# Kernel optimization log

Hardware: AMD Instinct MI355X
Metric: run time of the kernel (lower is better)

## Reference

```python
import jax, jax.numpy as jnp
from jax import lax
import numpy as np

B, S, E = 512, 128, 300
NF = 100          # filters per kernel size
NUM_CLASSES = 5


def setup_inputs() -> dict:
    key = jax.random.key(0)
    ks = jax.random.split(key, 9)
    def w(k, shape, fan_in):
        bound = 1.0 / np.sqrt(fan_in)
        return jax.random.uniform(k, shape, jnp.float32, -bound, bound)
    return {
        "x":   jax.random.normal(ks[0], (B, 1, S, E), jnp.float32),
        # conv weights: [out_ch=NF, in_ch=1, kh, kw=E] (the 100 separate 1-channel
        # convs of each kernel size are stacked into one grouped weight tensor)
        "w3": w(ks[1], (NF, 1, 3, E), 3 * E),
        "b3": w(ks[2], (NF,), 3 * E),
        "w4": w(ks[3], (NF, 1, 4, E), 4 * E),
        "b4": w(ks[4], (NF,), 4 * E),
        "w5": w(ks[5], (NF, 1, 5, E), 5 * E),
        "b5": w(ks[6], (NF,), 5 * E),
        "Wfc": w(ks[7], (NUM_CLASSES, 3 * NF), 3 * NF),
        "bfc": w(ks[8], (NUM_CLASSES,), 3 * NF),
    }


def _branch(x, w, b, pad):
    # conv over [B,1,S,E] with kernel [NF,1,k,E]; width fully consumed -> out [B,NF,S',1]
    y = lax.conv_general_dilated(
        x, w, window_strides=(1, 1), padding=[(pad, pad), (0, 0)],
        dimension_numbers=("NCHW", "OIHW", "NCHW"))
    y = jax.nn.relu(y + b[None, :, None, None])
    # relu then global max-pool over the length dim == max over (S', 1)
    return jnp.max(y, axis=(2, 3))  # [B, NF]


def reference(x, w3, b3, w4, b4, w5, b5, Wfc, bfc):
    feats = jnp.concatenate(
        [_branch(x, w3, b3, 0),   # k=3, no padding
         _branch(x, w4, b4, 1),   # k=4, padding (1,0)
         _branch(x, w5, b5, 2)],  # k=5, padding (2,0)
        axis=1)                   # [B, 300]
    logits = feats @ Wfc.T + bfc  # dropout is identity in eval mode
    return jax.nn.log_softmax(logits, axis=1)
```

## Files before the change

### kernel.cpp

```cpp
#include <hip/hip_runtime.h>

typedef __bf16 bf16x8 __attribute__((ext_vector_type(8)));
typedef float  f32x4  __attribute__((ext_vector_type(4)));
typedef unsigned short u16;

#define NB    512
#define SEQ   128
#define EMB   300

#define AROW 656
#define A_BYTES (69 * AROW)

#define PREP_TOT 430080
#define OFF_FEATS 876544

__device__ __forceinline__ u16 f2bf(float f) {
  unsigned u = __builtin_bit_cast(unsigned, f);
  return (u16)((u + 0x7fffu + ((u >> 16) & 1u)) >> 16);
}

__global__ void prep_weights(const float* __restrict__ w3, const float* __restrict__ w4,
                             const float* __restrict__ w5, u16* __restrict__ wu) {
  int idx = blockIdx.x * blockDim.x + threadIdx.x;
  if (idx >= PREP_TOT) return;
  const int cum[8]  = {0, 61440, 107520, 189440, 215040, 276480, 327680, 430080};
  const int ntwA[7] = {4, 3, 4, 1, 3, 2, 4};
  const int khA[7]  = {3, 3, 4, 5, 4, 5, 5};
  const int fl0A[7] = {0, 64, 0, 0, 64, 16, 48};
  int p = 0;
  #pragma unroll
  for (int q = 0; q < 6; ++q) if (idx >= cum[q + 1]) p = q + 1;
  int rem = idx - cum[p];
  int ntw = ntwA[p], kh = khA[p];
  int j = rem & 7, l = (rem >> 3) & 63, t = rem >> 9;
  int tloc = t % ntw, kt = t / ntw;
  int fl = fl0A[p] + tloc * 16 + (l & 15);
  int kk = kt * 32 + ((l >> 4) << 3) + j;
  int dk = kk / 320, e = kk - dk * 320;
  float v = 0.f;
  if (fl < 100 && e < 300) {
    if (kh == 3)      v = w3[(fl * 3 + dk) * 300 + e];
    else if (kh == 4) v = w4[(fl * 4 + dk) * 300 + e];
    else              v = w5[(fl * 5 + dk) * 300 + e];
  }
  wu[idx] = f2bf(v);
}

template<int NTW, int KH>
__device__ __forceinline__ void kloop_epi(const char* xs, const char* gstream,
                                          int l, int s0, int fl0,
                                          const float* __restrict__ bias, int sval,
                                          int foff, int b, float* __restrict__ feats) {
  const int lo = l & 15, hi = l >> 4;
  constexpr int DK0 = 5 - KH;

  f32x4 acc[4][NTW];
  #pragma unroll
  for (int mt = 0; mt < 4; ++mt)
    #pragma unroll
    for (int j = 0; j < NTW; ++j) acc[mt][j] = (f32x4){0.f, 0.f, 0.f, 0.f};

  bf16x8 aC[4], aN[4], b0[NTW], b1[NTW], b2[NTW], b3s[NTW];

  const char* gB = gstream + l * 16;
  #pragma unroll
  for (int j = 0; j < NTW; ++j) b0[j]  = *reinterpret_cast<const bf16x8*>(gB + j * 1024);
  gB += NTW * 1024;
  #pragma unroll
  for (int j = 0; j < NTW; ++j) b1[j]  = *reinterpret_cast<const bf16x8*>(gB + j * 1024);
  gB += NTW * 1024;
  #pragma unroll
  for (int j = 0; j < NTW; ++j) b2[j]  = *reinterpret_cast<const bf16x8*>(gB + j * 1024);
  gB += NTW * 1024;
  #pragma unroll
  for (int j = 0; j < NTW; ++j) b3s[j] = *reinterpret_cast<const bf16x8*>(gB + j * 1024);
  gB += NTW * 1024;

  int abase[4];
  #pragma unroll
  for (int mt = 0; mt < 4; ++mt) abase[mt] = (mt * 16 + lo + DK0) * AROW + hi * 16;

  #pragma unroll
  for (int mt = 0; mt < 4; ++mt)
    aC[mt] = *reinterpret_cast<const bf16x8*>(xs + abase[mt]);

#define STEP(AOFF, ACON, ANEX, BSET) {                                         \
    _Pragma("unroll") for (int mt = 0; mt < 4; ++mt)                           \
      ANEX[mt] = *reinterpret_cast<const bf16x8*>(xs + abase[mt] + (AOFF));    \
    __builtin_amdgcn_s_setprio(1);                                             \
    _Pragma("unroll") for (int mt = 0; mt < 4; ++mt)                           \
    _Pragma("unroll") for (int j = 0; j < NTW; ++j)                            \
      acc[mt][j] = __builtin_amdgcn_mfma_f32_16x16x32_bf16(ACON[mt], BSET[j],  \
                                                           acc[mt][j], 0, 0, 0); \
    __builtin_amdgcn_s_setprio(0);                                             \
    _Pragma("unroll") for (int j = 0; j < NTW; ++j)                            \
      BSET[j] = *reinterpret_cast<const bf16x8*>(gB + j * 1024);               \
    gB += NTW * 1024; }

#define BODY(SA, SB, SC, SD) {                                                 \
    STEP( 64, aC, aN, SA) STEP(128, aN, aC, SB) STEP(192, aC, aN, SC)          \
    STEP(256, aN, aC, SD) STEP(320, aC, aN, SA) STEP(384, aN, aC, SB)          \
    STEP(448, aC, aN, SC) STEP(512, aN, aC, SD) STEP(576, aC, aN, SA)          \
    STEP(656, aN, aC, SB)                                                      \
    _Pragma("unroll") for (int mt = 0; mt < 4; ++mt) abase[mt] += AROW; }

  BODY(b0, b1, b2, b3s)
  BODY(b2, b3s, b0, b1)
  BODY(b0, b1, b2, b3s)
  if constexpr (KH >= 4) { BODY(b2, b3s, b0, b1) }
  if constexpr (KH == 5) { BODY(b0, b1, b2, b3s) }
#undef BODY
#undef STEP

  #pragma unroll
  for (int j = 0; j < NTW; ++j) {
    int fl = fl0 + j * 16 + lo;
    if (fl < 100) {
      float bia  = bias[fl];
      float cmax = 0.f;
      #pragma unroll
      for (int mt = 0; mt < 4; ++mt)
        #pragma unroll
        for (int ii = 0; ii < 4; ++ii) {
          int s = s0 + mt * 16 + hi * 4 + ii;
          float v = acc[mt][j][ii] + bia;
          if (s < sval) cmax = fmaxf(cmax, v);
        }
      cmax = fmaxf(cmax, __shfl_xor(cmax, 16));
      cmax = fmaxf(cmax, __shfl_xor(cmax, 32));
      if (hi == 0)
        atomicMax((int*)&feats[b * 300 + foff + fl], __float_as_int(fmaxf(cmax, 0.f)));
    }
  }
}

__global__ __launch_bounds__(256, 2)
void conv_max_kernel(const float* __restrict__ x, const u16* __restrict__ wu,
                     const float* __restrict__ b3, const float* __restrict__ b4,
                     const float* __restrict__ b5, float* __restrict__ feats) {
  __shared__ __align__(16) char xs[A_BYTES];
  const int bid = blockIdx.x;
  const int b = bid >> 1, s0 = (bid & 1) * 64;
  const int tid = threadIdx.x;
  const int l = tid & 63, w = tid >> 6;
  const float* xb = x + (size_t)b * (SEQ * EMB);
  const char*  wB = (const char*)wu;

  for (int t = tid; t < 68 * 80; t += 256) {
    int r = t / 80, cg = t - r * 80;
    int xr = s0 - 2 + r;
    float4 v = make_float4(0.f, 0.f, 0.f, 0.f);
    if (xr >= 0 && xr < SEQ && cg < 75)
      v = *reinterpret_cast<const float4*>(xb + xr * EMB + cg * 4);
    ushort4 h;
    h.x = f2bf(v.x); h.y = f2bf(v.y); h.z = f2bf(v.z); h.w = f2bf(v.w);
    *reinterpret_cast<ushort4*>(xs + r * AROW + cg * 8) = h;
  }
  __syncthreads();

  if (w == 0) {
    kloop_epi<4, 3>(xs, wB + 0,      l, s0,  0, b3, 126,   0, b, feats);
    kloop_epi<3, 3>(xs, wB + 122880, l, s0, 64, b3, 126,   0, b, feats);
  } else if (w == 1) {
    kloop_epi<4, 4>(xs, wB + 215040, l, s0,  0, b4, 127, 100, b, feats);
    kloop_epi<1, 5>(xs, wB + 378880, l, s0,  0, b5, 128, 200, b, feats);
  } else if (w == 2) {
    kloop_epi<3, 4>(xs, wB + 430080, l, s0, 64, b4, 127, 100, b, feats);
    kloop_epi<2, 5>(xs, wB + 552960, l, s0, 16, b5, 128, 200, b, feats);
  } else {
    kloop_epi<4, 5>(xs, wB + 655360, l, s0, 48, b5, 128, 200, b, feats);
  }
}

__global__ void fc_kernel(const float* __restrict__ feats, const float* __restrict__ Wfc,
                          const float* __restrict__ bfc, float* __restrict__ out) {
  const int b = blockIdx.x, l = threadIdx.x;
  float acc[5] = {0.f, 0.f, 0.f, 0.f, 0.f};
  for (int e = l; e < 300; e += 64) {
    float fv = feats[b * 300 + e];
    #pragma unroll
    for (int c = 0; c < 5; ++c) acc[c] += fv * Wfc[c * 300 + e];
  }
  #pragma unroll
  for (int off = 32; off; off >>= 1) {
    #pragma unroll
    for (int c = 0; c < 5; ++c) acc[c] += __shfl_down(acc[c], off);
  }
  if (l == 0) {
    float lg[5], m = -1e30f;
    #pragma unroll
    for (int c = 0; c < 5; ++c) { lg[c] = acc[c] + bfc[c]; m = fmaxf(m, lg[c]); }
    float se = 0.f;
    #pragma unroll
    for (int c = 0; c < 5; ++c) se += expf(lg[c] - m);
    float ls = logf(se);
    #pragma unroll
    for (int c = 0; c < 5; ++c) out[b * 5 + c] = lg[c] - m - ls;
  }
}

extern "C" void kernel_launch(void* const* d_in, const int* in_sizes, int n_in,
                              void* d_out, int out_size, void* d_ws, size_t ws_size,
                              hipStream_t stream) {
  const float* x   = (const float*)d_in[0];
  const float* w3  = (const float*)d_in[1];
  const float* b3  = (const float*)d_in[2];
  const float* w4  = (const float*)d_in[3];
  const float* b4  = (const float*)d_in[4];
  const float* w5  = (const float*)d_in[5];
  const float* b5  = (const float*)d_in[6];
  const float* Wfc = (const float*)d_in[7];
  const float* bfc = (const float*)d_in[8];
  float* out = (float*)d_out;

  u16*   wu    = (u16*)d_ws;
  float* feats = (float*)((char*)d_ws + OFF_FEATS);

  hipMemsetAsync(feats, 0, NB * 300 * sizeof(float), stream);

  prep_weights<<<(PREP_TOT + 255) / 256, 256, 0, stream>>>(w3, w4, w5, wu);
  conv_max_kernel<<<NB * 2, 256, 0, stream>>>(x, wu, b3, b4, b5, feats);
  fc_kernel<<<NB, 64, 0, stream>>>(feats, Wfc, bfc, out);
}
```

Measured before the change: 75.20 us.

## Split sequence into 32-row tiles, halve accumulators, double-buffer weights instead of quad

Each block now covers 32 sequence positions instead of 64, so the grid quadruples and each wave keeps only 2 M-tiles of accumulators. The weight prefetch pipeline drops from four register buffers to two, and launch bounds rise to 4 blocks per CU to raise occupancy. The cost is that every weight fragment is streamed from global/L2 twice as often per output row, there is less MFMA work per weight load, and the weight loads are prefetched less far ahead. More blocks also do extra halo loads and more atomicMax calls.

```diff
diff --git a/kernel.cpp b/kernel.cpp
--- a/kernel.cpp
+++ b/kernel.cpp
@@ -9,7 +9,7 @@
 #define EMB   300
 
 #define AROW 656
-#define A_BYTES (69 * AROW)
+#define A_BYTES (37 * AROW)
 
 #define PREP_TOT 430080
 #define OFF_FEATS 876544
@@ -54,41 +54,35 @@
   const int lo = l & 15, hi = l >> 4;
   constexpr int DK0 = 5 - KH;
 
-  f32x4 acc[4][NTW];
-  #pragma unroll
-  for (int mt = 0; mt < 4; ++mt)
+  f32x4 acc[2][NTW];
+  #pragma unroll
+  for (int mt = 0; mt < 2; ++mt)
     #pragma unroll
     for (int j = 0; j < NTW; ++j) acc[mt][j] = (f32x4){0.f, 0.f, 0.f, 0.f};
 
-  bf16x8 aC[4], aN[4], b0[NTW], b1[NTW], b2[NTW], b3s[NTW];
+  bf16x8 aC[2], aN[2], bC[NTW], bN[NTW];
 
   const char* gB = gstream + l * 16;
   #pragma unroll
-  for (int j = 0; j < NTW; ++j) b0[j]  = *reinterpret_cast<const bf16x8*>(gB + j * 1024);
+  for (int j = 0; j < NTW; ++j) bC[j] = *reinterpret_cast<const bf16x8*>(gB + j * 1024);
   gB += NTW * 1024;
   #pragma unroll
-  for (int j = 0; j < NTW; ++j) b1[j]  = *reinterpret_cast<const bf16x8*>(gB + j * 1024);
+  for (int j = 0; j < NTW; ++j) bN[j] = *reinterpret_cast<const bf16x8*>(gB + j * 1024);
   gB += NTW * 1024;
-  #pragma unroll
-  for (int j = 0; j < NTW; ++j) b2[j]  = *reinterpret_cast<const bf16x8*>(gB + j * 1024);
-  gB += NTW * 1024;
-  #pragma unroll
-  for (int j = 0; j < NTW; ++j) b3s[j] = *reinterpret_cast<const bf16x8*>(gB + j * 1024);
-  gB += NTW * 1024;
-
-  int abase[4];
-  #pragma unroll
-  for (int mt = 0; mt < 4; ++mt) abase[mt] = (mt * 16 + lo + DK0) * AROW + hi * 16;
-
-  #pragma unroll
-  for (int mt = 0; mt < 4; ++mt)
+
+  int abase[2];
+  #pragma unroll
+  for (int mt = 0; mt < 2; ++mt) abase[mt] = (mt * 16 + lo + DK0) * AROW + hi * 16;
+
+  #pragma unroll
+  for (int mt = 0; mt < 2; ++mt)
     aC[mt] = *reinterpret_cast<const bf16x8*>(xs + abase[mt]);
 
 #define STEP(AOFF, ACON, ANEX, BSET) {                                         \
-    _Pragma("unroll") for (int mt = 0; mt < 4; ++mt)                           \
+    _Pragma("unroll") for (int mt = 0; mt < 2; ++mt)                           \
       ANEX[mt] = *reinterpret_cast<const bf16x8*>(xs + abase[mt] + (AOFF));    \
     __builtin_amdgcn_s_setprio(1);                                             \
-    _Pragma("unroll") for (int mt = 0; mt < 4; ++mt)                           \
+    _Pragma("unroll") for (int mt = 0; mt < 2; ++mt)                           \
     _Pragma("unroll") for (int j = 0; j < NTW; ++j)                            \
       acc[mt][j] = __builtin_amdgcn_mfma_f32_16x16x32_bf16(ACON[mt], BSET[j],  \
                                                            acc[mt][j], 0, 0, 0); \
@@ -97,18 +91,18 @@
       BSET[j] = *reinterpret_cast<const bf16x8*>(gB + j * 1024);               \
     gB += NTW * 1024; }
 
-#define BODY(SA, SB, SC, SD) {                                                 \
-    STEP( 64, aC, aN, SA) STEP(128, aN, aC, SB) STEP(192, aC, aN, SC)          \
-    STEP(256, aN, aC, SD) STEP(320, aC, aN, SA) STEP(384, aN, aC, SB)          \
-    STEP(448, aC, aN, SC) STEP(512, aN, aC, SD) STEP(576, aC, aN, SA)          \
-    STEP(656, aN, aC, SB)                                                      \
-    _Pragma("unroll") for (int mt = 0; mt < 4; ++mt) abase[mt] += AROW; }
-
-  BODY(b0, b1, b2, b3s)
-  BODY(b2, b3s, b0, b1)
-  BODY(b0, b1, b2, b3s)
-  if constexpr (KH >= 4) { BODY(b2, b3s, b0, b1) }
-  if constexpr (KH == 5) { BODY(b0, b1, b2, b3s) }
+#define BODY() {                                                               \
+    STEP( 64, aC, aN, bC) STEP(128, aN, aC, bN) STEP(192, aC, aN, bC)          \
+    STEP(256, aN, aC, bN) STEP(320, aC, aN, bC) STEP(384, aN, aC, bN)          \
+    STEP(448, aC, aN, bC) STEP(512, aN, aC, bN) STEP(576, aC, aN, bC)          \
+    STEP(656, aN, aC, bN)                                                      \
+    _Pragma("unroll") for (int mt = 0; mt < 2; ++mt) abase[mt] += AROW; }
+
+  BODY()
+  BODY()
+  BODY()
+  if constexpr (KH >= 4) { BODY() }
+  if constexpr (KH == 5) { BODY() }
 #undef BODY
 #undef STEP
 
@@ -119,7 +113,7 @@
       float bia  = bias[fl];
       float cmax = 0.f;
       #pragma unroll
-      for (int mt = 0; mt < 4; ++mt)
+      for (int mt = 0; mt < 2; ++mt)
         #pragma unroll
         for (int ii = 0; ii < 4; ++ii) {
           int s = s0 + mt * 16 + hi * 4 + ii;
@@ -134,19 +128,19 @@
   }
 }
 
-__global__ __launch_bounds__(256, 2)
+__global__ __launch_bounds__(256, 4)
 void conv_max_kernel(const float* __restrict__ x, const u16* __restrict__ wu,
                      const float* __restrict__ b3, const float* __restrict__ b4,
                      const float* __restrict__ b5, float* __restrict__ feats) {
   __shared__ __align__(16) char xs[A_BYTES];
   const int bid = blockIdx.x;
-  const int b = bid >> 1, s0 = (bid & 1) * 64;
+  const int b = bid >> 2, s0 = (bid & 3) * 32;
   const int tid = threadIdx.x;
   const int l = tid & 63, w = tid >> 6;
   const float* xb = x + (size_t)b * (SEQ * EMB);
   const char*  wB = (const char*)wu;
 
-  for (int t = tid; t < 68 * 80; t += 256) {
+  for (int t = tid; t < 36 * 80; t += 256) {
     int r = t / 80, cg = t - r * 80;
     int xr = s0 - 2 + r;
     float4 v = make_float4(0.f, 0.f, 0.f, 0.f);
@@ -219,6 +213,6 @@
   hipMemsetAsync(feats, 0, NB * 300 * sizeof(float), stream);
 
   prep_weights<<<(PREP_TOT + 255) / 256, 256, 0, stream>>>(w3, w4, w5, wu);
-  conv_max_kernel<<<NB * 2, 256, 0, stream>>>(x, wu, b3, b4, b5, feats);
+  conv_max_kernel<<<NB * 4, 256, 0, stream>>>(x, wu, b3, b4, b5, feats);
   fc_kernel<<<NB, 64, 0, stream>>>(feats, Wfc, bfc, out);
 }
```

New measurement: 92.95 us. +23.6%, slower.
